# Optimization experiments

Hardware: AMD Instinct MI355X
Metric: run time of the kernel (lower is better)

## Reference

```python
import jax, jax.numpy as jnp
import numpy as np

NUM_CLASSES = 128
EMBED_DIM = 256
HIDDEN = 1024
NUM_LAYERS = 2
BATCH = 64
SEQ = 256


def _gru_layer(x_seq, h0, w_ih, w_hh, b_ih, b_hh):
    # x_seq: [S, B, I], h0: [B, H], w_ih: [3H, I], w_hh: [3H, H]
    gi = jnp.einsum('sbi,gi->sbg', x_seq, w_ih) + b_ih  # precompute input gates [S,B,3H]

    def step(h, gi_t):
        gh = h @ w_hh.T + b_hh
        gir, giz, gin = jnp.split(gi_t, 3, axis=-1)
        ghr, ghz, ghn = jnp.split(gh, 3, axis=-1)
        r = jax.nn.sigmoid(gir + ghr)
        z = jax.nn.sigmoid(giz + ghz)
        n = jnp.tanh(gin + r * ghn)
        h_new = (1.0 - z) * n + z * h
        return h_new, h_new

    hT, out = jax.lax.scan(step, h0, gi)
    return out, hT  # out: [S, B, H]


def setup_inputs() -> dict:
    key = jax.random.key(0)
    ks = jax.random.split(key, 12)
    s_e = 1.0 / np.sqrt(HIDDEN)
    inp = {
        'x': jax.random.randint(ks[0], (BATCH, SEQ), 0, NUM_CLASSES, dtype=jnp.int64),
        'hs': jnp.zeros((NUM_LAYERS, BATCH, HIDDEN), dtype=jnp.float32),
        'embed': jax.random.normal(ks[1], (NUM_CLASSES, EMBED_DIM), dtype=jnp.float32),
        'w_ih0': jax.random.uniform(ks[2], (3 * HIDDEN, EMBED_DIM), minval=-s_e, maxval=s_e, dtype=jnp.float32),
        'w_hh0': jax.random.uniform(ks[3], (3 * HIDDEN, HIDDEN), minval=-s_e, maxval=s_e, dtype=jnp.float32),
        'b_ih0': jax.random.uniform(ks[4], (3 * HIDDEN,), minval=-s_e, maxval=s_e, dtype=jnp.float32),
        'b_hh0': jax.random.uniform(ks[5], (3 * HIDDEN,), minval=-s_e, maxval=s_e, dtype=jnp.float32),
        'w_ih1': jax.random.uniform(ks[6], (3 * HIDDEN, HIDDEN), minval=-s_e, maxval=s_e, dtype=jnp.float32),
        'w_hh1': jax.random.uniform(ks[7], (3 * HIDDEN, HIDDEN), minval=-s_e, maxval=s_e, dtype=jnp.float32),
        'b_ih1': jax.random.uniform(ks[8], (3 * HIDDEN,), minval=-s_e, maxval=s_e, dtype=jnp.float32),
        'b_hh1': jax.random.uniform(ks[9], (3 * HIDDEN,), minval=-s_e, maxval=s_e, dtype=jnp.float32),
        'w_proj': jax.random.uniform(ks[10], (NUM_CLASSES, HIDDEN), minval=-s_e, maxval=s_e, dtype=jnp.float32),
        'b_proj': jax.random.uniform(ks[11], (NUM_CLASSES,), minval=-s_e, maxval=s_e, dtype=jnp.float32),
    }
    return inp


def reference(x, hs, embed, w_ih0, w_hh0, b_ih0, b_hh0, w_ih1, w_hh1, b_ih1, b_hh1, w_proj, b_proj):
    # embedding lookup: [B, S] -> [B, S, E] -> time-major [S, B, E]
    word_embed = embed[x].transpose(1, 0, 2)
    out0, h0T = _gru_layer(word_embed, hs[0], w_ih0, w_hh0, b_ih0, b_hh0)
    out1, h1T = _gru_layer(out0, hs[1], w_ih1, w_hh1, b_ih1, b_hh1)
    # projection: [S, B, H] -> [S, B, C]
    logits = jnp.einsum('sbh,ch->sbc', out1, w_proj) + b_proj
    # permute back to batch-major and flatten: [B*S, C]
    logits = logits.transpose(1, 0, 2).reshape(-1, NUM_CLASSES)
    hT = jnp.stack([h0T, h1T], axis=0)
    return logits, hT
```

## Files before the change

kernel.cpp:

```cpp
#include <hip/hip_runtime.h>
#include <hip/hip_bf16.h>

#define SEQ    256
#define BATCH  64
#define EMB    256
#define HID    1024
#define GATES  3072
#define NCLS   128
#define TCH    16
#define ROWS   (TCH * BATCH)
#define NCH    (SEQ / TCH)
#define MX     (ROWS / 64)

typedef __attribute__((ext_vector_type(8))) short bf16x8;
typedef __attribute__((ext_vector_type(4))) float f32x4;

__device__ inline unsigned short f2bf(float x) {
    union { float f; unsigned int u; } v; v.f = x;
    v.u += 0x7fffu + ((v.u >> 16) & 1u);
    return (unsigned short)(v.u >> 16);
}

__global__ void conv_all(const float* __restrict__ emb, const float* __restrict__ wih0,
                         const float* __restrict__ whh0, const float* __restrict__ wih1,
                         const float* __restrict__ whh1, const float* __restrict__ wproj,
                         const float* __restrict__ hs,
                         unsigned short* __restrict__ embB, unsigned short* __restrict__ wih0B,
                         unsigned short* __restrict__ whh0B, unsigned short* __restrict__ wih1B,
                         unsigned short* __restrict__ whh1B, unsigned short* __restrict__ wprojB,
                         unsigned short* __restrict__ h0b0, unsigned short* __restrict__ h1b0,
                         float* __restrict__ h0f, float* __restrict__ h1f) {
    int i = (blockIdx.x * 256 + threadIdx.x) * 4;
    const float* src; unsigned short* dst; int off;
    if (i < 32768)         { src = emb;   dst = embB;   off = 0; }
    else if (i < 819200)   { src = wih0;  dst = wih0B;  off = 32768; }
    else if (i < 3964928)  { src = whh0;  dst = whh0B;  off = 819200; }
    else if (i < 7110656)  { src = wih1;  dst = wih1B;  off = 3964928; }
    else if (i < 10256384) { src = whh1;  dst = whh1B;  off = 7110656; }
    else if (i < 10387456) { src = wproj; dst = wprojB; off = 10256384; }
    else                   { src = hs;    dst = nullptr; off = 10387456; }
    int k = i - off;
    float4 v = *(const float4*)(src + k);
    if (dst) {
        dst[k + 0] = f2bf(v.x); dst[k + 1] = f2bf(v.y);
        dst[k + 2] = f2bf(v.z); dst[k + 3] = f2bf(v.w);
    } else {
        int kk = k & 65535;
        unsigned short* hb = (k < 65536) ? h0b0 : h1b0;
        float*          hf = (k < 65536) ? h0f  : h1f;
        int b = kk >> 10, j = kk & 1023;
        int bi = ((b >> 4) * 64 + (j >> 4)) * 256 + (b & 15) * 16 + (j & 15);
        hb[bi + 0] = f2bf(v.x); hb[bi + 1] = f2bf(v.y);
        hb[bi + 2] = f2bf(v.z); hb[bi + 3] = f2bf(v.w);
        hf[kk + 0] = v.x; hf[kk + 1] = v.y; hf[kk + 2] = v.z; hf[kk + 3] = v.w;
    }
}

template <int MODE, int KTOT>
__device__ __forceinline__ void gemm_dev(const unsigned short* __restrict__ A,
                                         const unsigned short* __restrict__ Bw,
                                         const float* __restrict__ bias,
                                         float* __restrict__ Cout, int N,
                                         const int* __restrict__ xidx,
                                         const unsigned short* __restrict__ emb,
                                         int row_base, int bx, int by,
                                         unsigned short* smem) {
    const int tid = threadIdx.x;
    const int w = tid >> 6, l = tid & 63;
    const int m0 = bx * 64, n0 = by * 64;
    const int r = l & 15;

    const unsigned short* apt[4];
    const unsigned short* bpt[4];
    int wrA[4], wrB[4];
#pragma unroll
    for (int i = 0; i < 4; ++i) {
        int u = tid + 256 * i;
        int row = u >> 4;
        int ku = u & 15;
        int slot = ku ^ (row & 7);
        if (MODE == 1) {
            int g = row_base + m0 + row;
            apt[i] = emb + (size_t)xidx[(g & 63) * SEQ + (g >> 6)] * KTOT + ku * 8;
        } else {
            apt[i] = A + (size_t)(m0 + row) * KTOT + ku * 8;
        }
        bpt[i] = Bw + (size_t)(n0 + row) * KTOT + ku * 8;
        wrA[i] = row * 128 + slot * 8;
        wrB[i] = 8192 + row * 128 + slot * 8;
    }

    f32x4 acc[4] = {};
    bf16x8 va[4], vb[4];

#pragma unroll
    for (int i = 0; i < 4; ++i) va[i] = *(const bf16x8*)(apt[i]);
#pragma unroll
    for (int i = 0; i < 4; ++i) vb[i] = *(const bf16x8*)(bpt[i]);

    constexpr int NKB = KTOT / 128;
#pragma unroll
    for (int kb = 0; kb < NKB; ++kb) {
#pragma unroll
        for (int i = 0; i < 4; ++i) *(bf16x8*)(smem + wrA[i]) = va[i];
#pragma unroll
        for (int i = 0; i < 4; ++i) *(bf16x8*)(smem + wrB[i]) = vb[i];
        __syncthreads();
        if (kb + 1 < NKB) {
            const int ko = (kb + 1) * 128;
#pragma unroll
            for (int i = 0; i < 4; ++i) va[i] = *(const bf16x8*)(apt[i] + ko);
#pragma unroll
            for (int i = 0; i < 4; ++i) vb[i] = *(const bf16x8*)(bpt[i] + ko);
        }
#pragma unroll
        for (int ks = 0; ks < 4; ++ks) {
            const int slot = (ks * 4 + (l >> 4)) ^ (r & 7);
            bf16x8 a = *(const bf16x8*)(smem + (w * 16 + r) * 128 + slot * 8);
#pragma unroll
            for (int nt = 0; nt < 4; ++nt) {
                bf16x8 b = *(const bf16x8*)(smem + 8192 + (nt * 16 + r) * 128 + slot * 8);
                acc[nt] = __builtin_amdgcn_mfma_f32_16x16x32_bf16(a, b, acc[nt], 0, 0, 0);
            }
        }
        __syncthreads();
    }

    const int la = l & 15, rbase = (l >> 4) * 4;
#pragma unroll
    for (int nt = 0; nt < 4; ++nt) {
        int colg = n0 + nt * 16 + la;
        float bsv = bias[colg];
#pragma unroll
        for (int i = 0; i < 4; ++i) {
            int rowg = m0 + w * 16 + rbase + i;
            float v = acc[nt][i] + bsv;
            if (MODE == 2) {
                int g = row_base + rowg;
                int s = g >> 6, b = g & 63;
                Cout[((size_t)(b * SEQ + s)) * NCLS + colg] = v;
            } else {
                Cout[(size_t)rowg * N + colg] = v;
            }
        }
    }
}

__global__ __launch_bounds__(256)
void gemm_multi(int na, int nb,
                const int* __restrict__ x, const unsigned short* __restrict__ embB,
                const unsigned short* __restrict__ wih0B, const float* __restrict__ bih0,
                float* __restrict__ giA, int rbA,
                const unsigned short* __restrict__ out0b,
                const unsigned short* __restrict__ wih1B, const float* __restrict__ bih1,
                float* __restrict__ giB,
                const unsigned short* __restrict__ out1b,
                const unsigned short* __restrict__ wprojB, const float* __restrict__ bproj,
                float* __restrict__ logits, int rbP) {
    __shared__ unsigned short smem[16384];
    int bid = blockIdx.x;
    if (bid < na) {
        gemm_dev<1, EMB>(nullptr, wih0B, bih0, giA, GATES, x, embB, rbA,
                         bid % MX, bid / MX, smem);
    } else if (bid < na + nb) {
        int b = bid - na;
        gemm_dev<0, HID>(out0b, wih1B, bih1, giB, GATES, nullptr, nullptr, 0,
                         b % MX, b / MX, smem);
    } else {
        int b = bid - na - nb;
        gemm_dev<2, HID>(out1b, wprojB, bproj, logits, NCLS, nullptr, nullptr, rbP,
                         b % MX, b / MX, smem);
    }
}

__global__ __launch_bounds__(256, 2)
void gru_dual(int n0,
              const float* __restrict__ gi0, const unsigned short* __restrict__ wh0,
              const float* __restrict__ bh0, float* __restrict__ h0f,
              unsigned short* __restrict__ h0p, unsigned short* __restrict__ h0q,
              unsigned short* __restrict__ out0, int* __restrict__ bar0,
              const float* __restrict__ gi1, const unsigned short* __restrict__ wh1,
              const float* __restrict__ bh1, float* __restrict__ h1f,
              unsigned short* __restrict__ h1p, unsigned short* __restrict__ h1q,
              unsigned short* __restrict__ out1, int* __restrict__ bar1) {
    __shared__ char smem[35840];
    float* sg = (float*)(smem + 32768);

    const int bid = blockIdx.x;
    const bool L1 = (bid >= n0);
    const int lb = L1 ? bid - n0 : bid;
    const float* gi = L1 ? gi1 : gi0;
    const unsigned short* whb = L1 ? wh1 : wh0;
    const float* b_hh = L1 ? bh1 : bh0;
    float* h_f = L1 ? h1f : h0f;
    const unsigned short* hbuf[2] = {L1 ? h1p : h0p, L1 ? h1q : h0q};
    unsigned short* outseq = L1 ? out1 : out0;
    int* bar = L1 ? bar1 : bar0;

    const int bg = lb >> 6;
    const int jt = lb & 63;
    const int b0 = bg * 16, j0 = jt * 16;
    const int tid = threadIdx.x;
    const int w = tid >> 6, l = tid & 63;

    bf16x8 wreg[32];
    if (w < 3) {
        const unsigned short* wrow = whb + (size_t)(w * HID + j0 + (l & 15)) * HID
                                     + ((l >> 4) * 8);
#pragma unroll
        for (int ks = 0; ks < 32; ++ks) wreg[ks] = *(const bf16x8*)(wrow + ks * 32);
    }

    const int prow = tid >> 4, pcol = tid & 15;
    const int pb = b0 + prow, pj = j0 + pcol;
    float hp = h_f[(size_t)pb * HID + pj];
    const float bhr = b_hh[pj], bhz = b_hh[HID + pj], bhn = b_hh[2 * HID + pj];

    const int rr = (tid >> 1) & 15;
    const int swr = (rr & 7) << 4;
    char* hdst = smem + rr * 2048 +
                 ((((tid >> 5) << 5) + ((tid & 1) << 4)) ^ swr);

    for (int t = 0; t < TCH; ++t) {
        const unsigned short* hin = hbuf[t & 1];
        unsigned short* hout = (unsigned short*)hbuf[(t + 1) & 1];

        const float* git = gi + ((size_t)(t * BATCH + pb)) * GATES;
        float gir = git[pj];
        float giz = git[HID + pj];
        float gin = git[2 * HID + pj];

        {
            const unsigned short* s0 = hin + ((size_t)bg << 14) + tid * 8;
            bf16x8 h0v, h1v, h2v, h3v, h4v, h5v, h6v, h7v;
            asm volatile(
                "global_load_dwordx4 %0, %8, off sc0 sc1\n\t"
                "global_load_dwordx4 %1, %9, off sc0 sc1\n\t"
                "global_load_dwordx4 %2, %10, off sc0 sc1\n\t"
                "global_load_dwordx4 %3, %11, off sc0 sc1\n\t"
                "global_load_dwordx4 %4, %12, off sc0 sc1\n\t"
                "global_load_dwordx4 %5, %13, off sc0 sc1\n\t"
                "global_load_dwordx4 %6, %14, off sc0 sc1\n\t"
                "global_load_dwordx4 %7, %15, off sc0 sc1"
                : "=&v"(h0v), "=&v"(h1v), "=&v"(h2v), "=&v"(h3v),
                  "=&v"(h4v), "=&v"(h5v), "=&v"(h6v), "=&v"(h7v)
                : "v"(s0), "v"(s0 + 2048), "v"(s0 + 4096), "v"(s0 + 6144),
                  "v"(s0 + 8192), "v"(s0 + 10240), "v"(s0 + 12288), "v"(s0 + 14336));
            asm volatile("s_waitcnt vmcnt(0)" ::: "memory");
            __builtin_amdgcn_sched_barrier(0);
            *(bf16x8*)(hdst + 0 * 256) = h0v; *(bf16x8*)(hdst + 1 * 256) = h1v;
            *(bf16x8*)(hdst + 2 * 256) = h2v; *(bf16x8*)(hdst + 3 * 256) = h3v;
            *(bf16x8*)(hdst + 4 * 256) = h4v; *(bf16x8*)(hdst + 5 * 256) = h5v;
            *(bf16x8*)(hdst + 6 * 256) = h6v; *(bf16x8*)(hdst + 7 * 256) = h7v;
        }
        __syncthreads();

        if (w < 3) {
            const int r = l & 15;
            const int sw = (r & 7) << 4;
            const int kq = (l >> 4) * 16;
            const int hbyte = r * 2048;
            f32x4 acc = {};
#pragma unroll
            for (int ks = 0; ks < 32; ++ks) {
                bf16x8 a = *(const bf16x8*)(smem + hbyte + ((ks * 64 + kq) ^ sw));
                acc = __builtin_amdgcn_mfma_f32_16x16x32_bf16(a, wreg[ks], acc, 0, 0, 0);
            }
            const int col = l & 15, rbase = (l >> 4) * 4;
#pragma unroll
            for (int i = 0; i < 4; ++i) sg[w * 256 + (rbase + i) * 16 + col] = acc[i];
        }
        __syncthreads();

        float ghr = sg[0 * 256 + tid] + bhr;
        float ghz = sg[1 * 256 + tid] + bhz;
        float ghn = sg[2 * 256 + tid] + bhn;
        float rr2 = 1.f / (1.f + __expf(-(gir + ghr)));
        float zz = 1.f / (1.f + __expf(-(giz + ghz)));
        float nn = tanhf(gin + rr2 * ghn);
        hp = (1.f - zz) * nn + zz * hp;
        unsigned short hb = f2bf(hp);
        outseq[((size_t)(t * BATCH + pb)) * HID + pj] = hb;

        *(unsigned short*)(smem + tid * 2) = hb;
        __syncthreads();

        if (tid < 32) {
            bf16x8 pk = *(const bf16x8*)(smem + tid * 16);
            unsigned short* dstp = hout + ((size_t)(bg * 64 + jt) << 8) + tid * 8;
            asm volatile(
                "global_store_dwordx4 %0, %1, off sc0 sc1\n\t"
                "s_waitcnt vmcnt(0)"
                :: "v"(dstp), "v"(pk) : "memory");
        }

        if (t < TCH - 1) {
            if (tid == 0) {
                __hip_atomic_store(bar + (((bg << 6) | jt) << 4), t + 1,
                                   __ATOMIC_RELAXED, __HIP_MEMORY_SCOPE_AGENT);
            }
            if (tid < 64) {
                const int* f = bar + (((bg << 6) | tid) << 4);
                while (!__all(__hip_atomic_load(f, __ATOMIC_RELAXED,
                                                __HIP_MEMORY_SCOPE_AGENT) > t)) {
                    __builtin_amdgcn_s_sleep(1);
                }
            }
            __syncthreads();
        }
    }

    h_f[(size_t)pb * HID + pj] = hp;
}

extern "C" void kernel_launch(void* const* d_in, const int* in_sizes, int n_in,
                              void* d_out, int out_size, void* d_ws, size_t ws_size,
                              hipStream_t stream) {
    const int*   x      = (const int*)d_in[0];
    const float* hs     = (const float*)d_in[1];
    const float* emb    = (const float*)d_in[2];
    const float* w_ih0  = (const float*)d_in[3];
    const float* w_hh0  = (const float*)d_in[4];
    const float* b_ih0  = (const float*)d_in[5];
    const float* b_hh0  = (const float*)d_in[6];
    const float* w_ih1  = (const float*)d_in[7];
    const float* w_hh1  = (const float*)d_in[8];
    const float* b_ih1  = (const float*)d_in[9];
    const float* b_hh1  = (const float*)d_in[10];
    const float* w_proj = (const float*)d_in[11];
    const float* b_proj = (const float*)d_in[12];

    float* logits = (float*)d_out;
    float* hT     = logits + (size_t)SEQ * BATCH * NCLS;

    char* p = (char*)d_ws;
    float* giA = (float*)p;                     p += (size_t)ROWS * GATES * 4;
    float* giB = (float*)p;                     p += (size_t)ROWS * GATES * 4;
    float* h0f = (float*)p;                     p += 65536 * 4;
    float* h1f = (float*)p;                     p += 65536 * 4;
    unsigned short* h0b0 = (unsigned short*)p;  p += 65536 * 2;
    unsigned short* h0b1 = (unsigned short*)p;  p += 65536 * 2;
    unsigned short* h1b0 = (unsigned short*)p;  p += 65536 * 2;
    unsigned short* h1b1 = (unsigned short*)p;  p += 65536 * 2;
    unsigned short* out0b = (unsigned short*)p; p += (size_t)ROWS * HID * 2;
    unsigned short* out1b[2];
    out1b[0] = (unsigned short*)p;              p += (size_t)ROWS * HID * 2;
    out1b[1] = (unsigned short*)p;              p += (size_t)ROWS * HID * 2;
    unsigned short* embB  = (unsigned short*)p; p += (size_t)NCLS * EMB * 2;
    unsigned short* wih0B = (unsigned short*)p; p += (size_t)GATES * EMB * 2;
    unsigned short* whh0B = (unsigned short*)p; p += (size_t)GATES * HID * 2;
    unsigned short* wih1B = (unsigned short*)p; p += (size_t)GATES * HID * 2;
    unsigned short* whh1B = (unsigned short*)p; p += (size_t)GATES * HID * 2;
    unsigned short* wprojB = (unsigned short*)p; p += (size_t)NCLS * HID * 2;
    int* bar = (int*)p;                         p += (size_t)32 * 4096 * 4;

    hipMemsetAsync(bar, 0, (size_t)32 * 4096 * 4, stream);

    conv_all<<<10272, 256, 0, stream>>>(emb, w_ih0, w_hh0, w_ih1, w_hh1, w_proj, hs,
                                        embB, wih0B, whh0B, wih1B, whh1B, wprojB,
                                        h0b0, h1b0, h0f, h1f);

    for (int c = 0; c < NCH; ++c) {
        int na = 768;
        int nb = (c >= 1) ? 768 : 0;
        int np = (c >= 2) ? 32 : 0;
        gemm_multi<<<na + nb + np, 256, 0, stream>>>(na, nb,
            x, embB, wih0B, b_ih0, giA, c * ROWS,
            out0b, wih1B, b_ih1, giB,
            out1b[(c - 2) & 1], wprojB, b_proj, logits, (c >= 2) ? (c - 2) * ROWS : 0);

        int grid = (c >= 1) ? 512 : 256;
        int c1 = (c >= 1) ? c - 1 : 0;
        gru_dual<<<grid, 256, 0, stream>>>(256,
            giA, whh0B, b_hh0, h0f, h0b0, h0b1, out0b, bar + (size_t)c * 4096,
            giB, whh1B, b_hh1, h1f, h1b0, h1b1, out1b[c1 & 1],
            bar + (size_t)(16 + c1) * 4096);
    }

    gemm_multi<<<768 + 32, 256, 0, stream>>>(0, 768,
        x, embB, wih0B, b_ih0, giA, 0,
        out0b, wih1B, b_ih1, giB,
        out1b[0], wprojB, b_proj, logits, 14 * ROWS);

    gru_dual<<<256, 256, 0, stream>>>(0,
        giA, whh0B, b_hh0, h0f, h0b0, h0b1, out0b, bar,
        giB, whh1B, b_hh1, h1f, h1b0, h1b1, out1b[1],
        bar + (size_t)31 * 4096);

    gemm_multi<<<32, 256, 0, stream>>>(0, 0,
        x, embB, wih0B, b_ih0, giA, 0,
        out0b, wih1B, b_ih1, giB,
        out1b[1], wprojB, b_proj, logits, 15 * ROWS);

    hipMemcpyAsync(hT, h0f, 65536 * 4, hipMemcpyDeviceToDevice, stream);
    hipMemcpyAsync(hT + 65536, h1f, 65536 * 4, hipMemcpyDeviceToDevice, stream);
}
```

Measured before the change: 1.526 ms.

## Fuse recurrent GRU steps with next-chunk input GEMMs in one pipelined kernel

Merges the recurrent GRU blocks and the input-gate and projection GEMM blocks into a single 'mega' kernel launch per pipeline stage. The gate and hidden-output buffers are double-buffered so the next chunk's GEMMs can run while the current chunk's recurrence executes. This is meant to remove the serialization between GEMM launches and recurrence launches and to fill idle CUs during the latency-bound recurrence. In exchange it needs extra workspace, falling back to the old schedule when the workspace is small. It also risks GEMM blocks competing with the spin-barrier GRU blocks for CU residency.

```diff
diff --git a/kernel.cpp b/kernel.cpp
--- a/kernel.cpp
+++ b/kernel.cpp
@@ -173,29 +173,12 @@
     }
 }
 
-__global__ __launch_bounds__(256, 2)
-void gru_dual(int n0,
-              const float* __restrict__ gi0, const unsigned short* __restrict__ wh0,
-              const float* __restrict__ bh0, float* __restrict__ h0f,
-              unsigned short* __restrict__ h0p, unsigned short* __restrict__ h0q,
-              unsigned short* __restrict__ out0, int* __restrict__ bar0,
-              const float* __restrict__ gi1, const unsigned short* __restrict__ wh1,
-              const float* __restrict__ bh1, float* __restrict__ h1f,
-              unsigned short* __restrict__ h1p, unsigned short* __restrict__ h1q,
-              unsigned short* __restrict__ out1, int* __restrict__ bar1) {
-    __shared__ char smem[35840];
+__device__ __forceinline__ void gru_body(int lb,
+        const float* __restrict__ gi, const unsigned short* __restrict__ whb,
+        const float* __restrict__ b_hh, float* __restrict__ h_f,
+        const unsigned short* __restrict__ hb0, const unsigned short* __restrict__ hb1,
+        unsigned short* __restrict__ outseq, int* __restrict__ bar, char* smem) {
     float* sg = (float*)(smem + 32768);
-
-    const int bid = blockIdx.x;
-    const bool L1 = (bid >= n0);
-    const int lb = L1 ? bid - n0 : bid;
-    const float* gi = L1 ? gi1 : gi0;
-    const unsigned short* whb = L1 ? wh1 : wh0;
-    const float* b_hh = L1 ? bh1 : bh0;
-    float* h_f = L1 ? h1f : h0f;
-    const unsigned short* hbuf[2] = {L1 ? h1p : h0p, L1 ? h1q : h0q};
-    unsigned short* outseq = L1 ? out1 : out0;
-    int* bar = L1 ? bar1 : bar0;
 
     const int bg = lb >> 6;
     const int jt = lb & 63;
@@ -215,6 +198,8 @@
     const int pb = b0 + prow, pj = j0 + pcol;
     float hp = h_f[(size_t)pb * HID + pj];
     const float bhr = b_hh[pj], bhz = b_hh[HID + pj], bhn = b_hh[2 * HID + pj];
+
+    const unsigned short* hbuf[2] = {hb0, hb1};
 
     const int rr = (tid >> 1) & 15;
     const int swr = (rr & 7) << 4;
@@ -313,6 +298,50 @@
     h_f[(size_t)pb * HID + pj] = hp;
 }
 
+__global__ __launch_bounds__(256, 2)
+void mega(int g0, int g1, int na, int nb, int np,
+          const float* __restrict__ gi0, const unsigned short* __restrict__ wh0,
+          const float* __restrict__ bh0, float* __restrict__ h0f,
+          unsigned short* __restrict__ h0p, unsigned short* __restrict__ h0q,
+          unsigned short* __restrict__ out0, int* __restrict__ bar0,
+          const float* __restrict__ gi1, const unsigned short* __restrict__ wh1,
+          const float* __restrict__ bh1, float* __restrict__ h1f,
+          unsigned short* __restrict__ h1p, unsigned short* __restrict__ h1q,
+          unsigned short* __restrict__ out1, int* __restrict__ bar1,
+          const int* __restrict__ x, const unsigned short* __restrict__ embB,
+          const unsigned short* __restrict__ wih0B, const float* __restrict__ bih0,
+          float* __restrict__ giA_nxt, int rbA,
+          const unsigned short* __restrict__ out0_prev,
+          const unsigned short* __restrict__ wih1B, const float* __restrict__ bih1,
+          float* __restrict__ giB_nxt,
+          const unsigned short* __restrict__ out1_old,
+          const unsigned short* __restrict__ wprojB, const float* __restrict__ bproj,
+          float* __restrict__ logits, int rbP) {
+    __shared__ char smem[35840];
+    const int bid = blockIdx.x;
+    const int ng = g0 + g1;
+    if (bid < ng) {
+        if (bid < g0)
+            gru_body(bid, gi0, wh0, bh0, h0f, h0p, h0q, out0, bar0, smem);
+        else
+            gru_body(bid - g0, gi1, wh1, bh1, h1f, h1p, h1q, out1, bar1, smem);
+    } else {
+        int b2 = bid - ng;
+        if (b2 < na) {
+            gemm_dev<1, EMB>(nullptr, wih0B, bih0, giA_nxt, GATES, x, embB, rbA,
+                             b2 % MX, b2 / MX, (unsigned short*)smem);
+        } else if (b2 < na + nb) {
+            int b = b2 - na;
+            gemm_dev<0, HID>(out0_prev, wih1B, bih1, giB_nxt, GATES, nullptr, nullptr, 0,
+                             b % MX, b / MX, (unsigned short*)smem);
+        } else {
+            int b = b2 - na - nb;
+            gemm_dev<2, HID>(out1_old, wprojB, bproj, logits, NCLS, nullptr, nullptr, rbP,
+                             b % MX, b / MX, (unsigned short*)smem);
+        }
+    }
+}
+
 extern "C" void kernel_launch(void* const* d_in, const int* in_sizes, int n_in,
                               void* d_out, int out_size, void* d_ws, size_t ws_size,
                               hipStream_t stream) {
@@ -333,16 +362,24 @@
     float* logits = (float*)d_out;
     float* hT     = logits + (size_t)SEQ * BATCH * NCLS;
 
+    const size_t GI_BYTES = (size_t)ROWS * GATES * 4;
+    const bool big = ws_size >= ((size_t)82 << 20);
+
     char* p = (char*)d_ws;
-    float* giA = (float*)p;                     p += (size_t)ROWS * GATES * 4;
-    float* giB = (float*)p;                     p += (size_t)ROWS * GATES * 4;
+    float* giA[2]; float* giB[2];
+    giA[0] = (float*)p; p += GI_BYTES;
+    giA[1] = big ? (float*)p : giA[0]; if (big) p += GI_BYTES;
+    giB[0] = (float*)p; p += GI_BYTES;
+    giB[1] = big ? (float*)p : giB[0]; if (big) p += GI_BYTES;
     float* h0f = (float*)p;                     p += 65536 * 4;
     float* h1f = (float*)p;                     p += 65536 * 4;
     unsigned short* h0b0 = (unsigned short*)p;  p += 65536 * 2;
     unsigned short* h0b1 = (unsigned short*)p;  p += 65536 * 2;
     unsigned short* h1b0 = (unsigned short*)p;  p += 65536 * 2;
     unsigned short* h1b1 = (unsigned short*)p;  p += 65536 * 2;
-    unsigned short* out0b = (unsigned short*)p; p += (size_t)ROWS * HID * 2;
+    unsigned short* out0b[2];
+    out0b[0] = (unsigned short*)p;              p += (size_t)ROWS * HID * 2;
+    out0b[1] = big ? (unsigned short*)p : out0b[0]; if (big) p += (size_t)ROWS * HID * 2;
     unsigned short* out1b[2];
     out1b[0] = (unsigned short*)p;              p += (size_t)ROWS * HID * 2;
     out1b[1] = (unsigned short*)p;              p += (size_t)ROWS * HID * 2;
@@ -360,37 +397,72 @@
                                         embB, wih0B, whh0B, wih1B, whh1B, wprojB,
                                         h0b0, h1b0, h0f, h1f);
 
-    for (int c = 0; c < NCH; ++c) {
-        int na = 768;
-        int nb = (c >= 1) ? 768 : 0;
-        int np = (c >= 2) ? 32 : 0;
-        gemm_multi<<<na + nb + np, 256, 0, stream>>>(na, nb,
-            x, embB, wih0B, b_ih0, giA, c * ROWS,
-            out0b, wih1B, b_ih1, giB,
-            out1b[(c - 2) & 1], wprojB, b_proj, logits, (c >= 2) ? (c - 2) * ROWS : 0);
-
-        int grid = (c >= 1) ? 512 : 256;
-        int c1 = (c >= 1) ? c - 1 : 0;
-        gru_dual<<<grid, 256, 0, stream>>>(256,
-            giA, whh0B, b_hh0, h0f, h0b0, h0b1, out0b, bar + (size_t)c * 4096,
-            giB, whh1B, b_hh1, h1f, h1b0, h1b1, out1b[c1 & 1],
-            bar + (size_t)(16 + c1) * 4096);
-    }
-
-    gemm_multi<<<768 + 32, 256, 0, stream>>>(0, 768,
-        x, embB, wih0B, b_ih0, giA, 0,
-        out0b, wih1B, b_ih1, giB,
-        out1b[0], wprojB, b_proj, logits, 14 * ROWS);
-
-    gru_dual<<<256, 256, 0, stream>>>(0,
-        giA, whh0B, b_hh0, h0f, h0b0, h0b1, out0b, bar,
-        giB, whh1B, b_hh1, h1f, h1b0, h1b1, out1b[1],
-        bar + (size_t)31 * 4096);
-
-    gemm_multi<<<32, 256, 0, stream>>>(0, 0,
-        x, embB, wih0B, b_ih0, giA, 0,
-        out0b, wih1B, b_ih1, giB,
-        out1b[1], wprojB, b_proj, logits, 15 * ROWS);
+    if (big) {
+        gemm_multi<<<768, 256, 0, stream>>>(768, 0,
+            x, embB, wih0B, b_ih0, giA[0], 0,
+            out0b[0], wih1B, b_ih1, giB[0],
+            out1b[0], wprojB, b_proj, logits, 0);
+
+        for (int k = 0; k < 18; ++k) {
+            int g0 = (k <= 15) ? 256 : 0;
+            int g1 = (k >= 2) ? 256 : 0;
+            int na = (k <= 14) ? 768 : 0;
+            int nb = (k >= 1 && k <= 16) ? 768 : 0;
+            int np = (k >= 3) ? 32 : 0;
+            int m = k - 2, n = k - 1, q = k - 3;
+            mega<<<g0 + g1 + na + nb + np, 256, 0, stream>>>(
+                g0, g1, na, nb, np,
+                giA[k & 1], whh0B, b_hh0, h0f, h0b0, h0b1, out0b[k & 1],
+                bar + (size_t)(k & 15) * 4096,
+                giB[m & 1], whh1B, b_hh1, h1f, h1b0, h1b1, out1b[m & 1],
+                bar + (size_t)(16 + (m & 15)) * 4096,
+                x, embB, wih0B, b_ih0, giA[(k + 1) & 1], (k + 1) * ROWS,
+                out0b[n & 1], wih1B, b_ih1, giB[n & 1],
+                out1b[q & 1], wprojB, b_proj, logits, q * ROWS);
+        }
+
+        gemm_multi<<<32, 256, 0, stream>>>(0, 0,
+            x, embB, wih0B, b_ih0, giA[0], 0,
+            out0b[0], wih1B, b_ih1, giB[0],
+            out1b[1], wprojB, b_proj, logits, 15 * ROWS);
+    } else {
+        for (int c = 0; c < NCH; ++c) {
+            int na = 768;
+            int nb = (c >= 1) ? 768 : 0;
+            int np = (c >= 2) ? 32 : 0;
+            gemm_multi<<<na + nb + np, 256, 0, stream>>>(na, nb,
+                x, embB, wih0B, b_ih0, giA[0], c * ROWS,
+                out0b[0], wih1B, b_ih1, giB[0],
+                out1b[(c - 2) & 1], wprojB, b_proj, logits,
+                (c >= 2) ? (c - 2) * ROWS : 0);
+
+            int g1 = (c >= 1) ? 256 : 0;
+            int c1 = (c >= 1) ? c - 1 : 0;
+            mega<<<256 + g1, 256, 0, stream>>>(256, g1, 0, 0, 0,
+                giA[0], whh0B, b_hh0, h0f, h0b0, h0b1, out0b[0],
+                bar + (size_t)c * 4096,
+                giB[0], whh1B, b_hh1, h1f, h1b0, h1b1, out1b[c1 & 1],
+                bar + (size_t)(16 + c1) * 4096,
+                x, embB, wih0B, b_ih0, giA[0], 0,
+                out0b[0], wih1B, b_ih1, giB[0],
+                out1b[0], wprojB, b_proj, logits, 0);
+        }
+        gemm_multi<<<768 + 32, 256, 0, stream>>>(0, 768,
+            x, embB, wih0B, b_ih0, giA[0], 0,
+            out0b[0], wih1B, b_ih1, giB[0],
+            out1b[0], wprojB, b_proj, logits, 14 * ROWS);
+        mega<<<256, 256, 0, stream>>>(0, 256, 0, 0, 0,
+            giA[0], whh0B, b_hh0, h0f, h0b0, h0b1, out0b[0], bar,
+            giB[0], whh1B, b_hh1, h1f, h1b0, h1b1, out1b[1],
+            bar + (size_t)31 * 4096,
+            x, embB, wih0B, b_ih0, giA[0], 0,
+            out0b[0], wih1B, b_ih1, giB[0],
+            out1b[0], wprojB, b_proj, logits, 0);
+        gemm_multi<<<32, 256, 0, stream>>>(0, 0,
+            x, embB, wih0B, b_ih0, giA[0], 0,
+            out0b[0], wih1B, b_ih1, giB[0],
+            out1b[1], wprojB, b_proj, logits, 15 * ROWS);
+    }
 
     hipMemcpyAsync(hT, h0f, 65536 * 4, hipMemcpyDeviceToDevice, stream);
     hipMemcpyAsync(hT + 65536, h1f, 65536 * 4, hipMemcpyDeviceToDevice, stream);
```

Result: no change. 1.527 ms (median of 2 runs) (+0.1%).
